# Kernel optimization log

Hardware: AMD Instinct MI355X
Metric: run time of the kernel (lower is better)

The kernel has to match this reference:

```python
import jax, jax.numpy as jnp
import numpy as np

N = 8192      # nodes
E = 262144    # edges (avg degree 32)
D_IN = 128    # feat dim (out_channels)
D_H = 256     # hidden_channels * 2
D_OUT = 64    # in_channels (final embedding dim)


def _sage_pool(feat, src, dst, n, Wp, bp, Ws, Wn, b, ew):
    # DGL SAGEConv('pool'): h_pool = relu(fc_pool(feat)); msg = h_pool[src] * ew;
    # h_neigh = max over in-edges (0 for isolated nodes);
    # out = fc_self(feat) + fc_neigh(h_neigh) + bias
    h = jax.nn.relu(feat @ Wp + bp)                          # [N, d_in]
    msg = h[src] * ew[:, None]                               # [E, d_in]
    agg = jax.ops.segment_max(msg, dst, num_segments=n)      # [N, d_in], -inf if no in-edges
    agg = jnp.where(jnp.isfinite(agg), agg, 0.0)
    return feat @ Ws + agg @ Wn + b


def setup_inputs() -> dict:
    key = jax.random.key(0)
    ks = jax.random.split(key, 20)
    feat = jax.random.normal(ks[0], (N, D_IN), dtype=jnp.float32)
    src = jax.random.randint(ks[1], (E,), 0, N)
    dst = jax.random.randint(ks[2], (E,), 0, N)
    edge_weight = jax.random.uniform(ks[3], (E,), dtype=jnp.float32)

    def lin(k, din, dout):
        return jax.random.normal(k, (din, dout), dtype=jnp.float32) / np.float32(np.sqrt(din))

    params = {}
    dims = [(D_IN, D_H), (D_H, D_H), (D_H, D_OUT)]
    i = 4
    for l, (di, do) in enumerate(dims, 1):
        params[f"Wp{l}"] = lin(ks[i], di, di); i += 1
        params[f"bp{l}"] = jnp.zeros((di,), jnp.float32)
        params[f"Ws{l}"] = lin(ks[i], di, do); i += 1
        params[f"Wn{l}"] = lin(ks[i], di, do); i += 1
        params[f"b{l}"] = jnp.zeros((do,), jnp.float32)

    return dict(feat=feat, src=src, dst=dst, edge_weight=edge_weight, n_nodes=N, **params)


def reference(feat, src, dst, edge_weight, n_nodes,
              Wp1, bp1, Ws1, Wn1, b1,
              Wp2, bp2, Ws2, Wn2, b2,
              Wp3, bp3, Ws3, Wn3, b3):
    hd = jax.nn.relu(_sage_pool(feat, src, dst, n_nodes, Wp1, bp1, Ws1, Wn1, b1, edge_weight))
    hd = jax.nn.relu(_sage_pool(hd,   src, dst, n_nodes, Wp2, bp2, Ws2, Wn2, b2, edge_weight))
    hd = jax.nn.relu(_sage_pool(hd,   src, dst, n_nodes, Wp3, bp3, Ws3, Wn3, b3, edge_weight))
    adj_rec = hd @ hd.T                                      # [N, N]
    return hd, adj_rec
```

## Files before the change

### kernel.cpp

```cpp
#include <hip/hip_runtime.h>
#include <hip/hip_bf16.h>

#define NN 8192
#define NE 262144
#define CAP 96
#define AWK 136

typedef __attribute__((ext_vector_type(8))) __bf16 bf16x8;
typedef __attribute__((ext_vector_type(4))) float f32x4;

__device__ __forceinline__ ushort f2b(float v) {
    __hip_bfloat16 b = __float2bfloat16(v);
    return *reinterpret_cast<ushort*>(&b);
}
__device__ __forceinline__ uint pack2(float lo, float hi) {
    return (uint)f2b(lo) | ((uint)f2b(hi) << 16);
}
__device__ __forceinline__ float b2f(ushort u) {
    return __uint_as_float(((uint)u) << 16);
}

template <bool A1F32, bool RELU, int OUTMODE, bool ADDC>
__device__ __forceinline__ void gemm_tile64(
    int by, int bx, const void* __restrict__ Av, const ushort* __restrict__ BT,
    int K, const float* __restrict__ bias, const ushort* __restrict__ cin,
    float* __restrict__ Cf, ushort* __restrict__ Cb, int N,
    ushort* As, ushort* Bs) {
    const int tid = threadIdx.x, lane = tid & 63, wave = tid >> 6;
    const int wm = (wave >> 1) * 32, wn = (wave & 1) * 32;
    const int r16 = lane & 15, kb = lane >> 4;
    const int m0 = by * 64, n0 = bx * 64;

    f32x4 acc[2][2];
#pragma unroll
    for (int i = 0; i < 2; ++i)
#pragma unroll
        for (int j = 0; j < 2; ++j) acc[i][j] = (f32x4)(0.f);

    for (int k0 = 0; k0 < K; k0 += 128) {
        if constexpr (A1F32) {
            const float* A = (const float*)Av;
#pragma unroll
            for (int rep = 0; rep < 8; ++rep) {
                int id = rep * 256 + tid;
                int row = id >> 5, c = id & 31;
                float4 f = *(const float4*)&A[(size_t)(m0 + row) * K + k0 + c * 4];
                uint2 o; o.x = pack2(f.x, f.y); o.y = pack2(f.z, f.w);
                *(uint2*)&As[row * AWK + c * 4] = o;
            }
        } else {
            const ushort* A = (const ushort*)Av;
#pragma unroll
            for (int rep = 0; rep < 4; ++rep) {
                int id = rep * 256 + tid;
                int row = id >> 4, c = id & 15;
                *(bf16x8*)&As[row * AWK + c * 8] =
                    *(const bf16x8*)&A[(size_t)(m0 + row) * K + k0 + c * 8];
            }
        }
#pragma unroll
        for (int rep = 0; rep < 4; ++rep) {
            int id = rep * 256 + tid;
            int row = id >> 4, c = id & 15;
            *(bf16x8*)&Bs[row * AWK + c * 8] =
                *(const bf16x8*)&BT[(size_t)(n0 + row) * K + k0 + c * 8];
        }
        __syncthreads();
#pragma unroll
        for (int kc = 0; kc < 4; ++kc) {
            bf16x8 a[2], b[2];
#pragma unroll
            for (int i = 0; i < 2; ++i)
                a[i] = *(const bf16x8*)&As[(wm + 16 * i + r16) * AWK + kc * 32 + kb * 8];
#pragma unroll
            for (int j = 0; j < 2; ++j)
                b[j] = *(const bf16x8*)&Bs[(wn + 16 * j + r16) * AWK + kc * 32 + kb * 8];
#pragma unroll
            for (int i = 0; i < 2; ++i)
#pragma unroll
                for (int j = 0; j < 2; ++j)
                    acc[i][j] = __builtin_amdgcn_mfma_f32_16x16x32_bf16(a[i], b[j], acc[i][j], 0, 0, 0);
        }
        __syncthreads();
    }

#pragma unroll
    for (int i = 0; i < 2; ++i) {
#pragma unroll
        for (int j = 0; j < 2; ++j) {
            int col = n0 + wn + 16 * j + r16;
            float bv = ADDC ? 0.f : bias[col];
#pragma unroll
            for (int r = 0; r < 4; ++r) {
                int row = m0 + wm + 16 * i + kb * 4 + r;
                float v = acc[i][j][r];
                if constexpr (ADDC) v += b2f(cin[(size_t)row * N + col]);
                else v += bv;
                if (RELU) v = fmaxf(v, 0.f);
                if (OUTMODE != 0) Cf[(size_t)row * N + col] = v;
                if (OUTMODE != 1) Cb[(size_t)row * N + col] = f2b(v);
            }
        }
    }
}

template <int DIN>
__device__ __forceinline__ void seg4(
    int grp, const ushort* __restrict__ Pin, const int* __restrict__ cnt,
    const uint2* __restrict__ slots, ushort* __restrict__ G) {
    constexpr int FPL = DIN / 64;
    const int lane = threadIdx.x & 63, wave = threadIdx.x >> 6;
    int node = grp * 4 + wave;
    int f0 = lane * FPL;
    int n = cnt[node]; if (n > CAP) n = CAP;
    const uint2* sl = &slots[(size_t)node * CAP];
    float mx[FPL];
#pragma unroll
    for (int i = 0; i < FPL; ++i) mx[i] = 0.f;
    auto upd = [&](uint s, float w) {
        const uint* hp = (const uint*)&Pin[(size_t)s * DIN + f0];
#pragma unroll
        for (int c = 0; c < FPL / 2; ++c) {
            uint u = hp[c];
            float lo = __uint_as_float(u << 16);
            float hi = __uint_as_float(u & 0xffff0000u);
            mx[2 * c] = fmaxf(mx[2 * c], lo * w);
            mx[2 * c + 1] = fmaxf(mx[2 * c + 1], hi * w);
        }
    };
    int e = 0;
    for (; e + 8 <= n; e += 8) {
        uint2 d[8];
#pragma unroll
        for (int t = 0; t < 8; ++t) d[t] = sl[e + t];
#pragma unroll
        for (int t = 0; t < 8; ++t) upd(d[t].x, __uint_as_float(d[t].y));
    }
    for (; e < n; ++e) { uint2 d = sl[e]; upd(d.x, __uint_as_float(d.y)); }
    uint* gp = (uint*)&G[(size_t)node * DIN + f0];
#pragma unroll
    for (int c = 0; c < FPL / 2; ++c) gp[c] = pack2(mx[2 * c], mx[2 * c + 1]);
}

struct PrepArgs {
    int* cnt;
    const float* w[9]; ushort* wt[9];
};

__global__ __launch_bounds__(256) void prep_k(PrepArgs a) {
    const int bid = blockIdx.x, tid = threadIdx.x;
    if (bid < 32) { a.cnt[bid * 256 + tid] = 0; return; }
    int id = (bid - 32) * 256 + tid;
    if (id >= 376832) return;
    const int cum[10] = {0, 16384, 49152, 81920, 147456, 212992, 278528, 344064, 360448, 376832};
    const int KK[9] = {128, 128, 128, 256, 256, 256, 256, 256, 256};
    const int LN[9] = {7, 8, 8, 8, 8, 8, 8, 6, 6};
    int m = 0;
#pragma unroll
    for (int t = 1; t < 9; ++t) m += (id >= cum[t]);
    int local = id - cum[m];
    int K = KK[m], ln = LN[m];
    int k = local >> ln, n = local & ((1 << ln) - 1);
    a.wt[m][n * K + k] = f2b(a.w[m][local]);
}

__global__ __launch_bounds__(256, 4) void scat_pool1_k(
    const int* __restrict__ src, const int* __restrict__ dst,
    const float* __restrict__ ew, int* __restrict__ cnt, uint2* __restrict__ slots,
    const float* __restrict__ feat, const ushort* __restrict__ WpT,
    const float* __restrict__ bp, ushort* __restrict__ P) {
    __shared__ __align__(16) ushort As[64 * AWK];
    __shared__ __align__(16) ushort Bs[64 * AWK];
    const int g = blockIdx.x / 5, r = blockIdx.x % 5;
    if (r == 4) {
        gemm_tile64<true, true, 0, false>(g >> 1, g & 1, feat, WpT, 128,
                                          bp, nullptr, nullptr, P, 128, As, Bs);
    } else {
        int e = (g * 4 + r) * 256 + threadIdx.x;
        int d = dst[e];
        int p = atomicAdd(&cnt[d], 1);
        if (p < CAP) slots[(size_t)d * CAP + p] = make_uint2((uint)src[e], __float_as_uint(ew[e]));
    }
}

template <int DIN, int RATIO, bool A1F32, int KSELF, int NSELF>
__global__ __launch_bounds__(256, 4) void seg_self_k(
    const ushort* __restrict__ Pin, const int* __restrict__ cnt,
    const uint2* __restrict__ slots, ushort* __restrict__ G,
    const void* __restrict__ Av, const ushort* __restrict__ WsT,
    const float* __restrict__ bias, ushort* __restrict__ Cs) {
    __shared__ __align__(16) ushort As[64 * AWK];
    __shared__ __align__(16) ushort Bs[64 * AWK];
    const int g = blockIdx.x / (RATIO + 1), r = blockIdx.x % (RATIO + 1);
    if (r == RATIO) {
        constexpr int NBX = NSELF / 64;
        gemm_tile64<A1F32, false, 0, false>(g / NBX, g % NBX, Av, WsT, KSELF,
                                            bias, nullptr, nullptr, Cs, NSELF, As, Bs);
    } else {
        seg4<DIN>(g * RATIO + r, Pin, cnt, slots, G);
    }
}

template <bool A1F32, bool RELU, int OUTMODE, bool ADDC>
__global__ __launch_bounds__(256, 4) void gemm_k(
    const void* __restrict__ Av, const ushort* __restrict__ BT, int K,
    const float* __restrict__ bias, const ushort* __restrict__ cin,
    float* __restrict__ Cf, ushort* __restrict__ Cb, int N) {
    __shared__ __align__(16) ushort As[64 * AWK];
    __shared__ __align__(16) ushort Bs[64 * AWK];
    gemm_tile64<A1F32, RELU, OUTMODE, ADDC>(blockIdx.y, blockIdx.x, Av, BT, K,
                                            bias, cin, Cf, Cb, N, As, Bs);
}

__global__ __launch_bounds__(256) void aat_k(const ushort* __restrict__ H,
                                             float* __restrict__ C) {
    __shared__ __align__(16) ushort As[128 * 72];
    __shared__ __align__(16) ushort Bs[128 * 72];
    int tid = threadIdx.x, lane = tid & 63, wave = tid >> 6;
    int wm = (wave >> 1) * 64, wn = (wave & 1) * 64;
    int r16 = lane & 15, kb = lane >> 4;
    int m0 = blockIdx.y * 128, n0 = blockIdx.x * 128;

#pragma unroll
    for (int rep = 0; rep < 4; ++rep) {
        int id = rep * 256 + tid;
        int row = id >> 3, c = id & 7;
        *(bf16x8*)&As[row * 72 + c * 8] = *(const bf16x8*)&H[(size_t)(m0 + row) * 64 + c * 8];
        *(bf16x8*)&Bs[row * 72 + c * 8] = *(const bf16x8*)&H[(size_t)(n0 + row) * 64 + c * 8];
    }
    __syncthreads();

    f32x4 acc[4][4];
#pragma unroll
    for (int i = 0; i < 4; ++i)
#pragma unroll
        for (int j = 0; j < 4; ++j) acc[i][j] = (f32x4)(0.f);

#pragma unroll
    for (int kc = 0; kc < 2; ++kc) {
        bf16x8 a[4], b[4];
#pragma unroll
        for (int i = 0; i < 4; ++i)
            a[i] = *(const bf16x8*)&As[(wm + 16 * i + r16) * 72 + kc * 32 + kb * 8];
#pragma unroll
        for (int j = 0; j < 4; ++j)
            b[j] = *(const bf16x8*)&Bs[(wn + 16 * j + r16) * 72 + kc * 32 + kb * 8];
#pragma unroll
        for (int i = 0; i < 4; ++i)
#pragma unroll
            for (int j = 0; j < 4; ++j)
                acc[i][j] = __builtin_amdgcn_mfma_f32_16x16x32_bf16(a[i], b[j], acc[i][j], 0, 0, 0);
    }

#pragma unroll
    for (int i = 0; i < 4; ++i) {
#pragma unroll
        for (int j = 0; j < 4; ++j) {
            int col = n0 + wn + 16 * j + r16;
#pragma unroll
            for (int r = 0; r < 4; ++r) {
                size_t row = m0 + wm + 16 * i + kb * 4 + r;
                C[row * NN + col] = acc[i][j][r];
            }
        }
    }
}

extern "C" void kernel_launch(void* const* d_in, const int* in_sizes, int n_in,
                              void* d_out, int out_size, void* d_ws, size_t ws_size,
                              hipStream_t stream) {
    const float* feat = (const float*)d_in[0];
    const int* src = (const int*)d_in[1];
    const int* dst = (const int*)d_in[2];
    const float* ew = (const float*)d_in[3];
    const float* Wp1 = (const float*)d_in[5];
    const float* bp1 = (const float*)d_in[6];
    const float* Ws1 = (const float*)d_in[7];
    const float* Wn1 = (const float*)d_in[8];
    const float* b1  = (const float*)d_in[9];
    const float* Wp2 = (const float*)d_in[10];
    const float* bp2 = (const float*)d_in[11];
    const float* Ws2 = (const float*)d_in[12];
    const float* Wn2 = (const float*)d_in[13];
    const float* b2  = (const float*)d_in[14];
    const float* Wp3 = (const float*)d_in[15];
    const float* bp3 = (const float*)d_in[16];
    const float* Ws3 = (const float*)d_in[17];
    const float* Wn3 = (const float*)d_in[18];
    const float* b3  = (const float*)d_in[19];

    float* out = (float*)d_out;
    float* adj = out + (size_t)NN * 64;

    char* ws = (char*)d_ws;
    int* cnt      = (int*)(ws + 0x0);
    uint2* slots  = (uint2*)(ws + 0x10000);
    ushort* Wp1T = (ushort*)(ws + 0x620000);
    ushort* Ws1T = (ushort*)(ws + 0x628000);
    ushort* Wn1T = (ushort*)(ws + 0x638000);
    ushort* Wp2T = (ushort*)(ws + 0x648000);
    ushort* Ws2T = (ushort*)(ws + 0x668000);
    ushort* Wn2T = (ushort*)(ws + 0x688000);
    ushort* Wp3T = (ushort*)(ws + 0x6A8000);
    ushort* Ws3T = (ushort*)(ws + 0x6C8000);
    ushort* Wn3T = (ushort*)(ws + 0x6D0000);
    ushort* P  = (ushort*)(ws + 0x700000);
    ushort* G  = (ushort*)(ws + 0xB00000);
    ushort* X  = (ushort*)(ws + 0xF00000);
    ushort* Y  = (ushort*)(ws + 0x1300000);
    ushort* Cs = (ushort*)(ws + 0x1700000);
    ushort* hdb = (ushort*)(ws + 0x1B00000);

    PrepArgs pa;
    pa.cnt = cnt;
    const float* wsrc[9] = {Wp1, Ws1, Wn1, Wp2, Ws2, Wn2, Wp3, Ws3, Wn3};
    ushort* wdst[9] = {Wp1T, Ws1T, Wn1T, Wp2T, Ws2T, Wn2T, Wp3T, Ws3T, Wn3T};
    for (int i = 0; i < 9; ++i) { pa.w[i] = wsrc[i]; pa.wt[i] = wdst[i]; }
    prep_k<<<32 + 1472, 256, 0, stream>>>(pa);

    scat_pool1_k<<<1280, 256, 0, stream>>>(src, dst, ew, cnt, slots, feat, Wp1T, bp1, P);

    seg_self_k<128, 4, true, 128, 256><<<2560, 256, 0, stream>>>(
        P, cnt, slots, G, feat, Ws1T, b1, Cs);
    gemm_k<false, true, 0, true><<<dim3(4, 128), 256, 0, stream>>>(
        G, Wn1T, 128, nullptr, Cs, nullptr, X, 256);

    gemm_k<false, true, 0, false><<<dim3(4, 128), 256, 0, stream>>>(
        X, Wp2T, 256, bp2, nullptr, nullptr, P, 256);
    seg_self_k<256, 4, false, 256, 256><<<2560, 256, 0, stream>>>(
        P, cnt, slots, G, X, Ws2T, b2, Cs);
    gemm_k<false, true, 0, true><<<dim3(4, 128), 256, 0, stream>>>(
        G, Wn2T, 256, nullptr, Cs, nullptr, Y, 256);

    gemm_k<false, true, 0, false><<<dim3(4, 128), 256, 0, stream>>>(
        Y, Wp3T, 256, bp3, nullptr, nullptr, P, 256);
    seg_self_k<256, 16, false, 256, 64><<<2176, 256, 0, stream>>>(
        P, cnt, slots, G, Y, Ws3T, b3, Cs);
    gemm_k<false, true, 2, true><<<dim3(1, 128), 256, 0, stream>>>(
        G, Wn3T, 256, nullptr, Cs, out, hdb, 64);

    aat_k<<<dim3(NN / 128, NN / 128), 256, 0, stream>>>(hdb, adj);
}
```

Before: 163.0 us.

## Shrink prep kernel and fold remaining weight transposes into scatter/pool kernel

```diff
diff --git a/kernel.cpp b/kernel.cpp
--- a/kernel.cpp
+++ b/kernel.cpp
@@ -142,44 +142,48 @@
     for (int c = 0; c < FPL / 2; ++c) gp[c] = pack2(mx[2 * c], mx[2 * c + 1]);
 }
 
-struct PrepArgs {
-    int* cnt;
-    const float* w[9]; ushort* wt[9];
+__global__ __launch_bounds__(256) void prep_k(int* cnt, const float* Wp1, ushort* Wp1T) {
+    const int bid = blockIdx.x, tid = threadIdx.x;
+    if (bid < 32) { cnt[bid * 256 + tid] = 0; return; }
+    int id = (bid - 32) * 256 + tid;
+    int k = id >> 7, n = id & 127;
+    Wp1T[n * 128 + k] = f2b(Wp1[id]);
+}
+
+struct SPArgs {
+    const int* src; const int* dst; const float* ew;
+    int* cnt; uint2* slots;
+    const float* feat; const ushort* WpT; const float* bp; ushort* P;
+    const float* w[8]; ushort* wt[8];
 };
 
-__global__ __launch_bounds__(256) void prep_k(PrepArgs a) {
-    const int bid = blockIdx.x, tid = threadIdx.x;
-    if (bid < 32) { a.cnt[bid * 256 + tid] = 0; return; }
-    int id = (bid - 32) * 256 + tid;
-    if (id >= 376832) return;
-    const int cum[10] = {0, 16384, 49152, 81920, 147456, 212992, 278528, 344064, 360448, 376832};
-    const int KK[9] = {128, 128, 128, 256, 256, 256, 256, 256, 256};
-    const int LN[9] = {7, 8, 8, 8, 8, 8, 8, 6, 6};
-    int m = 0;
-#pragma unroll
-    for (int t = 1; t < 9; ++t) m += (id >= cum[t]);
-    int local = id - cum[m];
-    int K = KK[m], ln = LN[m];
-    int k = local >> ln, n = local & ((1 << ln) - 1);
-    a.wt[m][n * K + k] = f2b(a.w[m][local]);
-}
-
-__global__ __launch_bounds__(256, 4) void scat_pool1_k(
-    const int* __restrict__ src, const int* __restrict__ dst,
-    const float* __restrict__ ew, int* __restrict__ cnt, uint2* __restrict__ slots,
-    const float* __restrict__ feat, const ushort* __restrict__ WpT,
-    const float* __restrict__ bp, ushort* __restrict__ P) {
+__global__ __launch_bounds__(256, 4) void scat_pool1_k(SPArgs a) {
     __shared__ __align__(16) ushort As[64 * AWK];
     __shared__ __align__(16) ushort Bs[64 * AWK];
-    const int g = blockIdx.x / 5, r = blockIdx.x % 5;
-    if (r == 4) {
-        gemm_tile64<true, true, 0, false>(g >> 1, g & 1, feat, WpT, 128,
-                                          bp, nullptr, nullptr, P, 128, As, Bs);
+    const int g = blockIdx.x / 21, r = blockIdx.x % 21;
+    if (r < 8) {
+        int e = (g * 8 + r) * 256 + threadIdx.x;
+        int d = a.dst[e];
+        int p = atomicAdd(&a.cnt[d], 1);
+        if (p < CAP) a.slots[(size_t)d * CAP + p] =
+            make_uint2((uint)a.src[e], __float_as_uint(a.ew[e]));
+    } else if (r < 10) {
+        int t = g * 2 + (r - 8);
+        gemm_tile64<true, true, 0, false>(t >> 1, t & 1, a.feat, a.WpT, 128,
+                                          a.bp, nullptr, nullptr, a.P, 128, As, Bs);
     } else {
-        int e = (g * 4 + r) * 256 + threadIdx.x;
-        int d = dst[e];
-        int p = atomicAdd(&cnt[d], 1);
-        if (p < CAP) slots[(size_t)d * CAP + p] = make_uint2((uint)src[e], __float_as_uint(ew[e]));
+        int id = (g * 11 + (r - 10)) * 256 + threadIdx.x;
+        if (id >= 360448) return;
+        const int cum[9] = {0, 32768, 65536, 131072, 196608, 262144, 327680, 344064, 360448};
+        const int KK[8] = {128, 128, 256, 256, 256, 256, 256, 256};
+        const int LN[8] = {8, 8, 8, 8, 8, 8, 6, 6};
+        int m = 0;
+#pragma unroll
+        for (int t = 1; t < 8; ++t) m += (id >= cum[t]);
+        int local = id - cum[m];
+        int K = KK[m], ln = LN[m];
+        int k = local >> ln, n = local & ((1 << ln) - 1);
+        a.wt[m][n * K + k] = f2b(a.w[m][local]);
     }
 }
 
@@ -311,14 +315,15 @@
     ushort* Cs = (ushort*)(ws + 0x1700000);
     ushort* hdb = (ushort*)(ws + 0x1B00000);
 
-    PrepArgs pa;
-    pa.cnt = cnt;
-    const float* wsrc[9] = {Wp1, Ws1, Wn1, Wp2, Ws2, Wn2, Wp3, Ws3, Wn3};
-    ushort* wdst[9] = {Wp1T, Ws1T, Wn1T, Wp2T, Ws2T, Wn2T, Wp3T, Ws3T, Wn3T};
-    for (int i = 0; i < 9; ++i) { pa.w[i] = wsrc[i]; pa.wt[i] = wdst[i]; }
-    prep_k<<<32 + 1472, 256, 0, stream>>>(pa);
-
-    scat_pool1_k<<<1280, 256, 0, stream>>>(src, dst, ew, cnt, slots, feat, Wp1T, bp1, P);
+    prep_k<<<96, 256, 0, stream>>>(cnt, Wp1, Wp1T);
+
+    SPArgs sa;
+    sa.src = src; sa.dst = dst; sa.ew = ew; sa.cnt = cnt; sa.slots = slots;
+    sa.feat = feat; sa.WpT = Wp1T; sa.bp = bp1; sa.P = P;
+    const float* wsrc[8] = {Ws1, Wn1, Wp2, Ws2, Wn2, Wp3, Ws3, Wn3};
+    ushort* wdst[8] = {Ws1T, Wn1T, Wp2T, Ws2T, Wn2T, Wp3T, Ws3T, Wn3T};
+    for (int i = 0; i < 8; ++i) { sa.w[i] = wsrc[i]; sa.wt[i] = wdst[i]; }
+    scat_pool1_k<<<128 * 21, 256, 0, stream>>>(sa);
 
     seg_self_k<128, 4, true, 128, 256><<<2560, 256, 0, stream>>>(
         P, cnt, slots, G, feat, Ws1T, b1, Cs);
```

New measurement: 163.9 us. Within noise of the previous version (+0.5%).
